# Kernel tuning notes

Hardware: AMD Instinct MI355X
Metric: run time of the kernel (lower is better)

The kernel has to match this reference:

```python
import jax, jax.numpy as jnp
import numpy as np

B, S, DM, H = 4, 1024, 1024, 16
D = DM // H  # attn_head_size = 64


def setup_inputs() -> dict:
    key = jax.random.key(0)
    ks = jax.random.split(key, 16)
    sc = 0.02
    return {
        "hidden_states": jax.random.normal(ks[0], (B, S, DM), jnp.float32),
        "wq": jax.random.normal(ks[1], (DM, DM), jnp.float32) * sc,
        "bq": jax.random.normal(ks[2], (DM,), jnp.float32) * sc,
        "wk": jax.random.normal(ks[3], (DM, DM), jnp.float32) * sc,
        "bk": jax.random.normal(ks[4], (DM,), jnp.float32) * sc,
        "wv": jax.random.normal(ks[5], (DM, DM), jnp.float32) * sc,
        "bv": jax.random.normal(ks[6], (DM,), jnp.float32) * sc,
        "wo": jax.random.normal(ks[7], (DM, DM), jnp.float32) * sc,
        "bo": jax.random.normal(ks[8], (DM,), jnp.float32) * sc,
        "wfq": jax.random.normal(ks[9], (DM, DM), jnp.float32) * sc,
        "bfq": jax.random.normal(ks[10], (DM,), jnp.float32) * sc,
        "wfg": jax.random.normal(ks[11], (DM, DM), jnp.float32) * sc,
        "bfg": jax.random.normal(ks[12], (DM,), jnp.float32) * sc,
        "up": jax.random.normal(ks[13], (H, 1, D), jnp.float32) * sc,
        "uz": jax.random.normal(ks[14], (H, 1, D), jnp.float32) * sc,
    }


def _split_heads(x):
    # [B, S, DM] -> [B, H, S, D]
    return x.reshape(x.shape[0], x.shape[1], H, D).transpose(0, 2, 1, 3)


def reference(hidden_states, wq, bq, wk, bk, wv, bv, wo, bo,
              wfq, bfq, wfg, bfg, up, uz):
    key_len = hidden_states.shape[1]
    mixed_q = hidden_states @ wq + bq  # [B, S, DM]
    mixed_k = hidden_states @ wk + bk
    mixed_v = hidden_states @ wv + bv

    # focus-attention Gaussian bias
    glo = jnp.mean(mixed_q, axis=1, keepdims=True)                      # [B, 1, DM]
    c = jnp.tanh((mixed_q @ wfq + bfq) + (glo @ wfg + bfg))             # [B, S, DM]
    c = _split_heads(c)                                                 # [B, H, S, D]
    p = jnp.sum(c * up[None], axis=-1)                                  # [B, H, S]
    z = jnp.sum(c * uz[None], axis=-1)                                  # [B, H, S]
    P = jax.nn.sigmoid(p) * key_len                                     # [B, H, S]
    Z = jax.nn.sigmoid(z) * key_len
    j = jnp.arange(key_len, dtype=P.dtype)                              # [S]
    # G[b,h,q,k] = -(k - P[b,h,q])^2 * 2 / Z[b,h,q]^2
    G = -((j[None, None, None, :] - P[..., None]) ** 2) * 2.0 / (Z[..., None] ** 2)

    q = _split_heads(mixed_q)
    k = _split_heads(mixed_k)
    v = _split_heads(mixed_v)

    scores = jnp.einsum("bhqd,bhkd->bhqk", q, k) / jnp.sqrt(jnp.float32(D))
    scores = scores + G
    probs = jax.nn.softmax(scores, axis=-1)  # dropout_prob = 0 -> no-op
    ctx = jnp.einsum("bhqk,bhkd->bhqd", probs, v)
    ctx = ctx.transpose(0, 2, 1, 3).reshape(ctx.shape[0], key_len, H * D)
    return ctx @ wo + bo
```

## Files before the change

### kernel.cpp

```cpp
#include <hip/hip_runtime.h>
#include <hip/hip_bf16.h>
#include <stdint.h>

#define DEV __device__ __forceinline__

typedef __attribute__((ext_vector_type(4))) float f32x4;
typedef __attribute__((ext_vector_type(8))) __bf16 bf16x8;
typedef __attribute__((ext_vector_type(4))) __bf16 bf16x4;
typedef __attribute__((ext_vector_type(4))) unsigned int uint4v;
typedef __attribute__((ext_vector_type(4))) int i32x4;

static constexpr int Bc = 4, Sc = 1024, DMc = 1024, Hc = 16, Dh = 64;
static constexpr int Mc = Bc * Sc;

DEV __bf16 f2b(float x) {
    unsigned u = __builtin_bit_cast(unsigned, x);
    unsigned r = (u + 0x7fffu + ((u >> 16) & 1u)) >> 16;
    return __builtin_bit_cast(__bf16, (unsigned short)r);
}
DEV float b2f(__bf16 x) {
    unsigned short s = __builtin_bit_cast(unsigned short, x);
    unsigned u = ((unsigned)s) << 16;
    return __builtin_bit_cast(float, u);
}
DEV unsigned cvt_pk_bf16(float a, float b) {
    unsigned r;
    asm("v_cvt_pk_bf16_f32 %0, %1, %2" : "=v"(r) : "v"(a), "v"(b));
    return r;
}
DEV void gload_lds16(const void* g, void* l) {
    __builtin_amdgcn_global_load_lds(
        (const __attribute__((address_space(1))) unsigned int*)g,
        (__attribute__((address_space(3))) unsigned int*)l,
        16, 0, 0);
}
DEV bf16x8 ldswz(const __bf16* base, int row, int cu) {
    const char* p = (const char*)base + row * 128 + (((cu) ^ (row & 7)) << 4);
    return *(const bf16x8*)p;
}

__global__ void k_cvt2(const float* __restrict__ hs, __bf16* __restrict__ hsb,
                       float* __restrict__ part0) {
    int sc = blockIdx.x, b = blockIdx.y, tid = threadIdx.x;
    int c0 = tid * 4;
    float4 s = {0.f, 0.f, 0.f, 0.f};
#pragma unroll
    for (int r = 0; r < 8; r++) {
        size_t row = (size_t)b * 1024 + sc * 8 + r;
        float4 v = *(const float4*)&hs[row * 1024 + c0];
        s.x += v.x; s.y += v.y; s.z += v.z; s.w += v.w;
        bf16x4 o = { f2b(v.x), f2b(v.y), f2b(v.z), f2b(v.w) };
        *(bf16x4*)&hsb[row * 1024 + c0] = o;
    }
    *(float4*)&part0[(size_t)(sc * 4 + b) * 1024 + c0] = s;
}

__global__ void k_tcvt5(const float* __restrict__ s0, const float* __restrict__ s1,
                        const float* __restrict__ s2, const float* __restrict__ s3,
                        const float* __restrict__ s4,
                        __bf16* __restrict__ d0, __bf16* __restrict__ d1,
                        __bf16* __restrict__ d2, __bf16* __restrict__ d3,
                        __bf16* __restrict__ d4, __bf16* __restrict__ wqb) {
    __shared__ float t[32][33];
    const float* in; __bf16* out;
    switch (blockIdx.z) {
        case 0: in = s0; out = d0; break;
        case 1: in = s1; out = d1; break;
        case 2: in = s2; out = d2; break;
        case 3: in = s3; out = d3; break;
        default: in = s4; out = d4; break;
    }
    int c0 = blockIdx.x * 32, r0 = blockIdx.y * 32;
    for (int j = 0; j < 4; j++) {
        float v = in[(size_t)(r0 + threadIdx.y + j * 8) * 1024 + c0 + threadIdx.x];
        t[threadIdx.y + j * 8][threadIdx.x] = v;
        if (blockIdx.z == 0)
            wqb[(size_t)(r0 + threadIdx.y + j * 8) * 1024 + c0 + threadIdx.x] = f2b(v);
    }
    __syncthreads();
    for (int j = 0; j < 4; j++)
        out[(size_t)(c0 + threadIdx.y + j * 8) * 1024 + r0 + threadIdx.x] = f2b(t[threadIdx.x][threadIdx.y + j * 8]);
}

template <int EPI, int BM>
__global__ __launch_bounds__(256) void k_gemm(
    const __bf16* __restrict__ A, const __bf16* __restrict__ Bt,
    const float* __restrict__ bias, void* __restrict__ Cout, int N, int K)
{
    constexpr int MF = BM / 32;
    constexpr int ACH = BM / 32;
    __shared__ __bf16 Al[2][BM * 64];
    __shared__ __bf16 Bl[2][128 * 64];
    const int bm = blockIdx.x, bn = blockIdx.y;
    const int tid = threadIdx.x, lane = tid & 63, wid = tid >> 6;
    const int l15 = lane & 15, lg = lane >> 4;
    const int qr = (wid >> 1) * (BM / 2), qc = (wid & 1) * 64;
    f32x4 acc[MF][4] = {};

    const __bf16* Ab = A + (size_t)bm * BM * K;
    const __bf16* Bb = Bt + (size_t)bn * 128 * K;

#pragma unroll
    for (int c = 0; c < ACH; c++) {
        int ch = c * 256 + tid, row = ch >> 3, cu = (ch & 7) ^ (row & 7);
        gload_lds16(&Ab[(size_t)row * K + cu * 8], &Al[0][ch * 8]);
    }
#pragma unroll
    for (int c = 0; c < 4; c++) {
        int ch = c * 256 + tid, row = ch >> 3, cu = (ch & 7) ^ (row & 7);
        gload_lds16(&Bb[(size_t)row * K + cu * 8], &Bl[0][ch * 8]);
    }
    asm volatile("s_waitcnt vmcnt(0)" ::: "memory");
    __builtin_amdgcn_s_barrier();

    int buf = 0;
    for (int t = 0; t < K / 64; t++) {
        if (t + 1 < K / 64) {
            int k0 = (t + 1) * 64;
#pragma unroll
            for (int c = 0; c < ACH; c++) {
                int ch = c * 256 + tid, row = ch >> 3, cu = (ch & 7) ^ (row & 7);
                gload_lds16(&Ab[(size_t)row * K + k0 + cu * 8], &Al[buf ^ 1][ch * 8]);
            }
#pragma unroll
            for (int c = 0; c < 4; c++) {
                int ch = c * 256 + tid, row = ch >> 3, cu = (ch & 7) ^ (row & 7);
                gload_lds16(&Bb[(size_t)row * K + k0 + cu * 8], &Bl[buf ^ 1][ch * 8]);
            }
        }
        bf16x8 af[MF][2], bfv[4][2];
#pragma unroll
        for (int m = 0; m < MF; m++)
#pragma unroll
            for (int ks = 0; ks < 2; ks++) af[m][ks] = ldswz(&Al[buf][0], qr + m * 16 + l15, ks * 4 + lg);
#pragma unroll
        for (int n = 0; n < 4; n++)
#pragma unroll
            for (int ks = 0; ks < 2; ks++) bfv[n][ks] = ldswz(&Bl[buf][0], qc + n * 16 + l15, ks * 4 + lg);
#pragma unroll
        for (int m = 0; m < MF; m++)
#pragma unroll
            for (int n = 0; n < 4; n++) {
                acc[m][n] = __builtin_amdgcn_mfma_f32_16x16x32_bf16(af[m][0], bfv[n][0], acc[m][n], 0, 0, 0);
                acc[m][n] = __builtin_amdgcn_mfma_f32_16x16x32_bf16(af[m][1], bfv[n][1], acc[m][n], 0, 0, 0);
            }
        asm volatile("s_waitcnt vmcnt(0)" ::: "memory");
        __builtin_amdgcn_s_barrier();
        buf ^= 1;
    }
#pragma unroll
    for (int m = 0; m < MF; m++) {
        int row_base = bm * BM + qr + m * 16 + lg * 4;
#pragma unroll
        for (int n = 0; n < 4; n++) {
            int col = bn * 128 + qc + n * 16 + l15;
            float bsum = bias ? bias[col] : 0.0f;
#pragma unroll
            for (int r = 0; r < 4; r++) {
                int row = row_base + r;
                float v = acc[m][n][r] + bsum;
                if constexpr (EPI == 2) ((float*)Cout)[(size_t)row * N + col] = v;
                else ((__bf16*)Cout)[(size_t)row * N + col] = f2b(v);
            }
        }
    }
}

__global__ __launch_bounds__(256) void k_qkvc(
    const __bf16* __restrict__ A, const __bf16* __restrict__ BtAll,
    const float* __restrict__ bq, const float* __restrict__ bk, const float* __restrict__ bv,
    const float* __restrict__ gt2, const float* __restrict__ up, const float* __restrict__ uz,
    __bf16* __restrict__ mq, __bf16* __restrict__ mk_, __bf16* __restrict__ vt,
    float* __restrict__ Pf, float* __restrict__ Zf)
{
    constexpr int K = 1024;
    __shared__ __bf16 Al[2][128 * 64];
    __shared__ __bf16 Bl[2][128 * 64];
    const int bm = blockIdx.x, bn = blockIdx.y;
    const int tid = threadIdx.x, lane = tid & 63, wid = tid >> 6;
    const int l15 = lane & 15, lg = lane >> 4;
    const int qr = (wid >> 1) * 64, qc = (wid & 1) * 64;
    f32x4 acc[4][4] = {};

    const __bf16* Ab = A + (size_t)bm * 128 * K;
    const __bf16* Bb = BtAll + (size_t)bn * 128 * K;

#pragma unroll
    for (int c = 0; c < 4; c++) {
        int ch = c * 256 + tid, row = ch >> 3, cu = (ch & 7) ^ (row & 7);
        gload_lds16(&Ab[(size_t)row * K + cu * 8], &Al[0][ch * 8]);
        gload_lds16(&Bb[(size_t)row * K + cu * 8], &Bl[0][ch * 8]);
    }
    asm volatile("s_waitcnt vmcnt(0)" ::: "memory");
    __builtin_amdgcn_s_barrier();

    int buf = 0;
    for (int t = 0; t < 16; t++) {
        if (t < 15) {
            int k0 = (t + 1) * 64;
#pragma unroll
            for (int c = 0; c < 4; c++) {
                int ch = c * 256 + tid, row = ch >> 3, cu = (ch & 7) ^ (row & 7);
                gload_lds16(&Ab[(size_t)row * K + k0 + cu * 8], &Al[buf ^ 1][ch * 8]);
                gload_lds16(&Bb[(size_t)row * K + k0 + cu * 8], &Bl[buf ^ 1][ch * 8]);
            }
        }
        bf16x8 af[4][2], bfv[4][2];
#pragma unroll
        for (int m = 0; m < 4; m++)
#pragma unroll
            for (int ks = 0; ks < 2; ks++) af[m][ks] = ldswz(&Al[buf][0], qr + m * 16 + l15, ks * 4 + lg);
#pragma unroll
        for (int n = 0; n < 4; n++)
#pragma unroll
            for (int ks = 0; ks < 2; ks++) bfv[n][ks] = ldswz(&Bl[buf][0], qc + n * 16 + l15, ks * 4 + lg);
#pragma unroll
        for (int m = 0; m < 4; m++)
#pragma unroll
            for (int n = 0; n < 4; n++) {
                acc[m][n] = __builtin_amdgcn_mfma_f32_16x16x32_bf16(af[m][0], bfv[n][0], acc[m][n], 0, 0, 0);
                acc[m][n] = __builtin_amdgcn_mfma_f32_16x16x32_bf16(af[m][1], bfv[n][1], acc[m][n], 0, 0, 0);
            }
        asm volatile("s_waitcnt vmcnt(0)" ::: "memory");
        __builtin_amdgcn_s_barrier();
        buf ^= 1;
    }

    const int chunk = bn >> 3;
    if (chunk == 3) {
        const int h = (bn & 7) * 2 + (qc >> 6);
        float upv[4], uzv[4];
#pragma unroll
        for (int n = 0; n < 4; n++) {
            upv[n] = up[h * 64 + n * 16 + l15];
            uzv[n] = uz[h * 64 + n * 16 + l15];
        }
#pragma unroll
        for (int m = 0; m < 4; m++) {
            int row_base = bm * 128 + qr + m * 16 + lg * 4;
#pragma unroll
            for (int r = 0; r < 4; r++) {
                int row = row_base + r;
                float p = 0.f, z = 0.f;
#pragma unroll
                for (int n = 0; n < 4; n++) {
                    int col = (bn & 7) * 128 + qc + n * 16 + l15;
                    float cv = tanhf(acc[m][n][r] + gt2[(row >> 10) * 1024 + col]);
                    p += cv * upv[n];
                    z += cv * uzv[n];
                }
#pragma unroll
                for (int d = 1; d < 16; d <<= 1) {
                    p += __shfl_xor(p, d, 16);
                    z += __shfl_xor(z, d, 16);
                }
                if (l15 == 0) {
                    int bb = row >> 10, s = row & 1023;
                    Pf[((size_t)(bb * 16 + h)) * 1024 + s] = 1024.f / (1.f + __expf(-p));
                    Zf[((size_t)(bb * 16 + h)) * 1024 + s] = 1024.f / (1.f + __expf(-z));
                }
            }
        }
    } else if (chunk == 2) {
        const int b = bm >> 3;
#pragma unroll
        for (int m = 0; m < 4; m++) {
            int s0 = (bm & 7) * 128 + qr + m * 16 + lg * 4;
#pragma unroll
            for (int n = 0; n < 4; n++) {
                int col = (bn & 7) * 128 + qc + n * 16 + l15;
                int h = col >> 6, d = col & 63;
                float bsum = bv[col];
                bf16x4 o = { f2b(acc[m][n][0] + bsum), f2b(acc[m][n][1] + bsum),
                             f2b(acc[m][n][2] + bsum), f2b(acc[m][n][3] + bsum) };
                *(bf16x4*)&vt[((size_t)((b * 16 + h) * 64 + d)) * 1024 + s0] = o;
            }
        }
    } else {
        const float* bias = chunk == 0 ? bq : bk;
        __bf16* outp = chunk == 0 ? mq : mk_;
#pragma unroll
        for (int m = 0; m < 4; m++) {
            int row_base = bm * 128 + qr + m * 16 + lg * 4;
#pragma unroll
            for (int n = 0; n < 4; n++) {
                int col = (bn & 7) * 128 + qc + n * 16 + l15;
                float bsum = bias[col];
#pragma unroll
                for (int r = 0; r < 4; r++) {
                    int row = row_base + r;
                    outp[(size_t)row * 1024 + col] = f2b(acc[m][n][r] + bsum);
                }
            }
        }
    }
}

__global__ void k_glo2(const float* __restrict__ part0, const float* __restrict__ wq,
                       float* __restrict__ glo_part) {
    __shared__ float ghs_l[256];
    int tid = threadIdx.x, kc = blockIdx.y;
    {
        int bb = tid >> 6, kk = tid & 63, k = kc * 64 + kk;
        float s = 0.f;
        for (int sc = 0; sc < 128; sc++) s += part0[(size_t)(sc * 4 + bb) * 1024 + k];
        ghs_l[tid] = s * (1.0f / 1024.f);
    }
    __syncthreads();
    int n = blockIdx.x * 256 + tid;
    float a0 = 0, a1 = 0, a2 = 0, a3 = 0;
    for (int j = 0; j < 64; j++) {
        float w = wq[(size_t)(kc * 64 + j) * 1024 + n];
        a0 += ghs_l[j] * w; a1 += ghs_l[64 + j] * w; a2 += ghs_l[128 + j] * w; a3 += ghs_l[192 + j] * w;
    }
    glo_part[(kc * 4 + 0) * 1024 + n] = a0;
    glo_part[(kc * 4 + 1) * 1024 + n] = a1;
    glo_part[(kc * 4 + 2) * 1024 + n] = a2;
    glo_part[(kc * 4 + 3) * 1024 + n] = a3;
}
__global__ void k_gt2p(const float* __restrict__ glo_part, const float* __restrict__ bq,
                       const float* __restrict__ wfg, const float* __restrict__ wfq,
                       float* __restrict__ gt_part) {
    __shared__ float glo_l[256];
    int tid = threadIdx.x, kc = blockIdx.y;
    {
        int bb = tid >> 6, kk = tid & 63, k = kc * 64 + kk;
        float s = bq[k];
        for (int k2 = 0; k2 < 16; k2++) s += glo_part[(k2 * 4 + bb) * 1024 + k];
        glo_l[tid] = s;
    }
    __syncthreads();
    int n = blockIdx.x * 256 + tid;
    float a0 = 0, a1 = 0, a2 = 0, a3 = 0, t = 0;
    for (int j = 0; j < 64; j++) {
        int k = kc * 64 + j;
        float wg = wfg[(size_t)k * 1024 + n];
        float wf = wfq[(size_t)k * 1024 + n];
        a0 += glo_l[j] * wg; a1 += glo_l[64 + j] * wg; a2 += glo_l[128 + j] * wg; a3 += glo_l[192 + j] * wg;
        t += bq[k] * wf;
    }
    gt_part[(kc * 4 + 0) * 1024 + n] = a0 + t;
    gt_part[(kc * 4 + 1) * 1024 + n] = a1 + t;
    gt_part[(kc * 4 + 2) * 1024 + n] = a2 + t;
    gt_part[(kc * 4 + 3) * 1024 + n] = a3 + t;
}
__global__ void k_red_gt(const float* __restrict__ gt_part, const float* __restrict__ bfg,
                         const float* __restrict__ bfq, float* __restrict__ gt2) {
    int i = blockIdx.x * 256 + threadIdx.x;
    int b = i >> 10, n = i & 1023;
    float s = bfg[n] + bfq[n];
    for (int kc = 0; kc < 16; kc++) s += gt_part[(kc * 4 + b) * 1024 + n];
    gt2[i] = s;
}

DEV bf16x8 ldfrag(const __bf16* base, int row, int colbyte) {
    const char* p = (const char*)base + (size_t)row * 128 + (colbyte ^ ((row & 7) << 4));
    return *(const bf16x8*)p;
}

__global__ __launch_bounds__(256) void k_attn(
    const __bf16* __restrict__ Q, const __bf16* __restrict__ Kx, const __bf16* __restrict__ Vt_g,
    const float* __restrict__ Pf, const float* __restrict__ Zf, __bf16* __restrict__ ctx)
{
    __shared__ __bf16 Kl[2][64 * 64];
    __shared__ __bf16 Vl[2][64 * 64];
    const int qt = blockIdx.x, h = blockIdx.y, b = blockIdx.z;
    const int tid = threadIdx.x, lane = tid & 63, wid = tid >> 6;
    const int l15 = lane & 15, lg = lane >> 4;
    const int qbase = qt * 128 + wid * 32;
    const size_t qoff = ((size_t)(b * Sc)) * DMc + h * Dh;

    bf16x8 qf[2][2];
#pragma unroll
    for (int qh = 0; qh < 2; qh++)
#pragma unroll
        for (int dh = 0; dh < 2; dh++)
            qf[qh][dh] = *(const bf16x8*)&Q[qoff + (size_t)(qbase + qh * 16 + l15) * DMc + dh * 32 + lg * 8];

    float Pr[2], Ar[2];
#pragma unroll
    for (int qh = 0; qh < 2; qh++) {
        int row = qbase + qh * 16 + l15;
        float pp = Pf[((size_t)(b * 16 + h)) * 1024 + row];
        float zz = Zf[((size_t)(b * 16 + h)) * 1024 + row];
        Pr[qh] = pp; Ar[qh] = 2.0f / (zz * zz);
    }
    float l[2] = {0.f, 0.f};
    f32x4 oacc[2][4] = {};

    const __bf16* Kbase = Kx + qoff;
    const __bf16* Vbase = Vt_g + ((size_t)((b * 16 + h) * 64)) * 1024;

#pragma unroll
    for (int i = 0; i < 2; i++) {
        int ch = i * 256 + tid, row = ch >> 3, off = ch & 7;
        uint4v kv = *(const uint4v*)&Kbase[(size_t)row * DMc + off * 8];
        uint4v vv = *(const uint4v*)&Vbase[(size_t)row * 1024 + off * 8];
        *(uint4v*)((char*)&Kl[0][0] + row * 128 + ((off * 16) ^ ((row & 7) << 4))) = kv;
        *(uint4v*)((char*)&Vl[0][0] + row * 128 + ((off * 16) ^ ((row & 7) << 4))) = vv;
    }
    __syncthreads();

    for (int t = 0; t < 16; t++) {
        const int buf = t & 1;
        uint4v rk[2], rv[2];
        if (t < 15) {
#pragma unroll
            for (int i = 0; i < 2; i++) {
                int ch = i * 256 + tid, row = ch >> 3, off = ch & 7;
                rk[i] = *(const uint4v*)&Kbase[(size_t)((t + 1) * 64 + row) * DMc + off * 8];
                rv[i] = *(const uint4v*)&Vbase[(size_t)row * 1024 + (t + 1) * 64 + off * 8];
            }
        }

        f32x4 st[2][4];
        __builtin_amdgcn_s_setprio(1);
#pragma unroll
        for (int c = 0; c < 4; c++) {
            bf16x8 kb0 = ldfrag(&Kl[buf][0], c * 16 + l15, lg * 16);
            bf16x8 kb1 = ldfrag(&Kl[buf][0], c * 16 + l15, 64 + lg * 16);
#pragma unroll
            for (int qh = 0; qh < 2; qh++) {
                f32x4 a = {0.f, 0.f, 0.f, 0.f};
                a = __builtin_amdgcn_mfma_f32_16x16x32_bf16(kb0, qf[qh][0], a, 0, 0, 0);
                a = __builtin_amdgcn_mfma_f32_16x16x32_bf16(kb1, qf[qh][1], a, 0, 0, 0);
                st[qh][c] = a;
            }
        }
        __builtin_amdgcn_s_setprio(0);

        int pk[2][4][2];
#pragma unroll
        for (int qh = 0; qh < 2; qh++) {
            float s[16];
#pragma unroll
            for (int c = 0; c < 4; c++)
#pragma unroll
                for (int r = 0; r < 4; r++) {
                    float kidx = (float)(t * 64 + c * 16 + lg * 4 + r);
                    float dk = kidx - Pr[qh];
                    s[c * 4 + r] = __expf(st[qh][c][r] * 0.125f - dk * dk * Ar[qh]);
                }
            float rs = 0.f;
#pragma unroll
            for (int i = 0; i < 16; i++) rs += s[i];
            rs += __shfl_xor(rs, 16, 64);
            rs += __shfl_xor(rs, 32, 64);
            l[qh] += rs;
#pragma unroll
            for (int c = 0; c < 4; c++) {
                pk[qh][c][0] = (int)cvt_pk_bf16(s[c * 4 + 0], s[c * 4 + 1]);
                pk[qh][c][1] = (int)cvt_pk_bf16(s[c * 4 + 2], s[c * 4 + 3]);
            }
        }

        const int a0 = (((lg & 1) << 1) * 16 + l15) * 4;
        const int a1 = a0 + 64;
        const int selhi = lg >> 1;
#pragma unroll
        for (int kh = 0; kh < 2; kh++) {
            bf16x8 vb[4];
#pragma unroll
            for (int dt = 0; dt < 4; dt++) vb[dt] = ldfrag(&Vl[buf][0], dt * 16 + l15, kh * 64 + lg * 16);
#pragma unroll
            for (int qh = 0; qh < 2; qh++) {
                int w[4];
#pragma unroll
                for (int wi = 0; wi < 4; wi++) {
                    int addr = (wi < 2) ? a0 : a1;
                    int pr = wi & 1;
                    int va = __builtin_amdgcn_ds_bpermute(addr, pk[qh][kh * 2 + 0][pr]);
                    int vb2 = __builtin_amdgcn_ds_bpermute(addr, pk[qh][kh * 2 + 1][pr]);
                    w[wi] = selhi ? vb2 : va;
                }
                i32x4 wv = {w[0], w[1], w[2], w[3]};
                bf16x8 pa = __builtin_bit_cast(bf16x8, wv);
                __builtin_amdgcn_s_setprio(1);
#pragma unroll
                for (int dt = 0; dt < 4; dt++)
                    oacc[qh][dt] = __builtin_amdgcn_mfma_f32_16x16x32_bf16(pa, vb[dt], oacc[qh][dt], 0, 0, 0);
                __builtin_amdgcn_s_setprio(0);
            }
        }

        if (t < 15) {
#pragma unroll
            for (int i = 0; i < 2; i++) {
                int ch = i * 256 + tid, row = ch >> 3, off = ch & 7;
                *(uint4v*)((char*)&Kl[buf ^ 1][0] + row * 128 + ((off * 16) ^ ((row & 7) << 4))) = rk[i];
                *(uint4v*)((char*)&Vl[buf ^ 1][0] + row * 128 + ((off * 16) ^ ((row & 7) << 4))) = rv[i];
            }
        }
        __syncthreads();
    }

#pragma unroll
    for (int qh = 0; qh < 2; qh++) {
        float lr[4];
#pragma unroll
        for (int r = 0; r < 4; r++) lr[r] = __shfl(l[qh], lg * 4 + r, 16);
#pragma unroll
        for (int dt = 0; dt < 4; dt++)
#pragma unroll
            for (int r = 0; r < 4; r++) {
                int row = qbase + qh * 16 + lg * 4 + r;
                ctx[((size_t)(b * Sc) + row) * DMc + h * Dh + dt * 16 + l15] =
                    f2b(oacc[qh][dt][r] / lr[r]);
            }
    }
}

extern "C" void kernel_launch(void* const* d_in, const int* in_sizes, int n_in,
                              void* d_out, int out_size, void* d_ws, size_t ws_size,
                              hipStream_t stream) {
    const float* hs  = (const float*)d_in[0];
    const float* wq  = (const float*)d_in[1];
    const float* bq  = (const float*)d_in[2];
    const float* wk  = (const float*)d_in[3];
    const float* bk  = (const float*)d_in[4];
    const float* wv  = (const float*)d_in[5];
    const float* bv  = (const float*)d_in[6];
    const float* wo  = (const float*)d_in[7];
    const float* bo  = (const float*)d_in[8];
    const float* wfq = (const float*)d_in[9];
    const float* bfq = (const float*)d_in[10];
    const float* wfg = (const float*)d_in[11];
    const float* bfg = (const float*)d_in[12];
    const float* up  = (const float*)d_in[13];
    const float* uz  = (const float*)d_in[14];

    char* ws = (char*)d_ws;
    const size_t MB = 1ull << 20;
    __bf16* hsb   = (__bf16*)(ws);
    __bf16* BtAll = (__bf16*)(ws + 8 * MB);
    __bf16* wfqT  = (__bf16*)(ws + 16 * MB);
    __bf16* woT   = (__bf16*)(ws + 18 * MB);
    __bf16* mq    = (__bf16*)(ws + 20 * MB);
    __bf16* mk    = (__bf16*)(ws + 28 * MB);
    __bf16* vt    = (__bf16*)(ws + 36 * MB);
    __bf16* ctxb  = (__bf16*)(ws);
    __bf16* wqb   = (__bf16*)(ws + 55 * MB);
    char* sm = ws + 52 * MB;
    float* Pf       = (float*)(sm);
    float* Zf       = (float*)(sm + (256 << 10));
    float* glo_part = (float*)(sm + (512 << 10));
    float* gt_part  = (float*)(sm + (768 << 10));
    float* gt2      = (float*)(sm + (1024 << 10));
    float* part0    = (float*)(ws + 57 * MB);

    k_cvt2<<<dim3(128, 4), 256, 0, stream>>>(hs, hsb, part0);
    k_tcvt5<<<dim3(32, 32, 5), dim3(32, 8), 0, stream>>>(
        wq, wk, wv, wfq, wo,
        BtAll, BtAll + 1048576, BtAll + 2097152, wfqT, woT, wqb);

    k_glo2<<<dim3(4, 16), 256, 0, stream>>>(part0, wq, glo_part);
    k_gt2p<<<dim3(4, 16), 256, 0, stream>>>(glo_part, bq, wfg, wfq, gt_part);
    k_red_gt<<<16, 256, 0, stream>>>(gt_part, bfg, bfq, gt2);

    k_gemm<0, 64><<<dim3(16, 8), 256, 0, stream>>>(wfqT, wqb, nullptr, BtAll + 3145728, DMc, DMc);

    k_qkvc<<<dim3(32, 32), 256, 0, stream>>>(hsb, BtAll, bq, bk, bv, gt2, up, uz,
                                             mq, mk, vt, Pf, Zf);

    k_attn<<<dim3(8, 16, 4), 256, 0, stream>>>(mq, mk, vt, Pf, Zf, ctxb);

    k_gemm<2, 64><<<dim3(64, 8), 256, 0, stream>>>(ctxb, woT, bo, d_out, DMc, DMc);
}
```

Measured before the change: 168.6 us.

## Double KV tile size per pipeline stage in attention kernel

```diff
diff --git a/kernel.cpp b/kernel.cpp
--- a/kernel.cpp
+++ b/kernel.cpp
@@ -353,8 +353,12 @@
     gt2[i] = s;
 }
 
-DEV bf16x8 ldfrag(const __bf16* base, int row, int colbyte) {
+DEV bf16x8 ldfragK(const __bf16* base, int row, int colbyte) {
     const char* p = (const char*)base + (size_t)row * 128 + (colbyte ^ ((row & 7) << 4));
+    return *(const bf16x8*)p;
+}
+DEV bf16x8 ldfragV(const __bf16* base, int row, int colbyte) {
+    const char* p = (const char*)base + (size_t)row * 256 + (colbyte ^ ((row & 15) << 4));
     return *(const bf16x8*)p;
 }
 
@@ -362,8 +366,8 @@
     const __bf16* __restrict__ Q, const __bf16* __restrict__ Kx, const __bf16* __restrict__ Vt_g,
     const float* __restrict__ Pf, const float* __restrict__ Zf, __bf16* __restrict__ ctx)
 {
-    __shared__ __bf16 Kl[2][64 * 64];
-    __shared__ __bf16 Vl[2][64 * 64];
+    __shared__ __bf16 Kl[2][128 * 64];
+    __shared__ __bf16 Vl[2][64 * 128];
     const int qt = blockIdx.x, h = blockIdx.y, b = blockIdx.z;
     const int tid = threadIdx.x, lane = tid & 63, wid = tid >> 6;
     const int l15 = lane & 15, lg = lane >> 4;
@@ -392,103 +396,117 @@
     const __bf16* Vbase = Vt_g + ((size_t)((b * 16 + h) * 64)) * 1024;
 
 #pragma unroll
-    for (int i = 0; i < 2; i++) {
-        int ch = i * 256 + tid, row = ch >> 3, off = ch & 7;
-        uint4v kv = *(const uint4v*)&Kbase[(size_t)row * DMc + off * 8];
-        uint4v vv = *(const uint4v*)&Vbase[(size_t)row * 1024 + off * 8];
-        *(uint4v*)((char*)&Kl[0][0] + row * 128 + ((off * 16) ^ ((row & 7) << 4))) = kv;
-        *(uint4v*)((char*)&Vl[0][0] + row * 128 + ((off * 16) ^ ((row & 7) << 4))) = vv;
+    for (int i = 0; i < 4; i++) {
+        int ch = i * 256 + tid;
+        {
+            int row = ch >> 3, off = ch & 7;
+            uint4v kv = *(const uint4v*)&Kbase[(size_t)row * DMc + off * 8];
+            *(uint4v*)((char*)&Kl[0][0] + row * 128 + ((off * 16) ^ ((row & 7) << 4))) = kv;
+        }
+        {
+            int row = ch >> 4, off = ch & 15;
+            uint4v vv = *(const uint4v*)&Vbase[(size_t)row * 1024 + off * 8];
+            *(uint4v*)((char*)&Vl[0][0] + row * 256 + ((off * 16) ^ ((row & 15) << 4))) = vv;
+        }
     }
     __syncthreads();
 
-    for (int t = 0; t < 16; t++) {
+    for (int t = 0; t < 8; t++) {
         const int buf = t & 1;
-        uint4v rk[2], rv[2];
-        if (t < 15) {
-#pragma unroll
-            for (int i = 0; i < 2; i++) {
-                int ch = i * 256 + tid, row = ch >> 3, off = ch & 7;
-                rk[i] = *(const uint4v*)&Kbase[(size_t)((t + 1) * 64 + row) * DMc + off * 8];
-                rv[i] = *(const uint4v*)&Vbase[(size_t)row * 1024 + (t + 1) * 64 + off * 8];
-            }
-        }
-
-        f32x4 st[2][4];
-        __builtin_amdgcn_s_setprio(1);
-#pragma unroll
-        for (int c = 0; c < 4; c++) {
-            bf16x8 kb0 = ldfrag(&Kl[buf][0], c * 16 + l15, lg * 16);
-            bf16x8 kb1 = ldfrag(&Kl[buf][0], c * 16 + l15, 64 + lg * 16);
+        uint4v rk[4], rv[4];
+        if (t < 7) {
+#pragma unroll
+            for (int i = 0; i < 4; i++) {
+                int ch = i * 256 + tid;
+                int krow = ch >> 3, koff = ch & 7;
+                rk[i] = *(const uint4v*)&Kbase[(size_t)((t + 1) * 128 + krow) * DMc + koff * 8];
+                int vrow = ch >> 4, voff = ch & 15;
+                rv[i] = *(const uint4v*)&Vbase[(size_t)vrow * 1024 + (t + 1) * 128 + voff * 8];
+            }
+        }
+
+#pragma unroll
+        for (int sub = 0; sub < 2; sub++) {
+            f32x4 st[2][4];
+            __builtin_amdgcn_s_setprio(1);
+#pragma unroll
+            for (int c = 0; c < 4; c++) {
+                bf16x8 kb0 = ldfragK(&Kl[buf][0], sub * 64 + c * 16 + l15, lg * 16);
+                bf16x8 kb1 = ldfragK(&Kl[buf][0], sub * 64 + c * 16 + l15, 64 + lg * 16);
+#pragma unroll
+                for (int qh = 0; qh < 2; qh++) {
+                    f32x4 a = {0.f, 0.f, 0.f, 0.f};
+                    a = __builtin_amdgcn_mfma_f32_16x16x32_bf16(kb0, qf[qh][0], a, 0, 0, 0);
+                    a = __builtin_amdgcn_mfma_f32_16x16x32_bf16(kb1, qf[qh][1], a, 0, 0, 0);
+                    st[qh][c] = a;
+                }
+            }
+            __builtin_amdgcn_s_setprio(0);
+
+            int pk[2][4][2];
 #pragma unroll
             for (int qh = 0; qh < 2; qh++) {
-                f32x4 a = {0.f, 0.f, 0.f, 0.f};
-                a = __builtin_amdgcn_mfma_f32_16x16x32_bf16(kb0, qf[qh][0], a, 0, 0, 0);
-                a = __builtin_amdgcn_mfma_f32_16x16x32_bf16(kb1, qf[qh][1], a, 0, 0, 0);
-                st[qh][c] = a;
-            }
-        }
-        __builtin_amdgcn_s_setprio(0);
-
-        int pk[2][4][2];
-#pragma unroll
-        for (int qh = 0; qh < 2; qh++) {
-            float s[16];
-#pragma unroll
-            for (int c = 0; c < 4; c++)
-#pragma unroll
-                for (int r = 0; r < 4; r++) {
-                    float kidx = (float)(t * 64 + c * 16 + lg * 4 + r);
-                    float dk = kidx - Pr[qh];
-                    s[c * 4 + r] = __expf(st[qh][c][r] * 0.125f - dk * dk * Ar[qh]);
-                }
-            float rs = 0.f;
-#pragma unroll
-            for (int i = 0; i < 16; i++) rs += s[i];
-            rs += __shfl_xor(rs, 16, 64);
-            rs += __shfl_xor(rs, 32, 64);
-            l[qh] += rs;
-#pragma unroll
-            for (int c = 0; c < 4; c++) {
-                pk[qh][c][0] = (int)cvt_pk_bf16(s[c * 4 + 0], s[c * 4 + 1]);
-                pk[qh][c][1] = (int)cvt_pk_bf16(s[c * 4 + 2], s[c * 4 + 3]);
-            }
-        }
-
-        const int a0 = (((lg & 1) << 1) * 16 + l15) * 4;
-        const int a1 = a0 + 64;
-        const int selhi = lg >> 1;
-#pragma unroll
-        for (int kh = 0; kh < 2; kh++) {
-            bf16x8 vb[4];
-#pragma unroll
-            for (int dt = 0; dt < 4; dt++) vb[dt] = ldfrag(&Vl[buf][0], dt * 16 + l15, kh * 64 + lg * 16);
-#pragma unroll
-            for (int qh = 0; qh < 2; qh++) {
-                int w[4];
-#pragma unroll
-                for (int wi = 0; wi < 4; wi++) {
-                    int addr = (wi < 2) ? a0 : a1;
-                    int pr = wi & 1;
-                    int va = __builtin_amdgcn_ds_bpermute(addr, pk[qh][kh * 2 + 0][pr]);
-                    int vb2 = __builtin_amdgcn_ds_bpermute(addr, pk[qh][kh * 2 + 1][pr]);
-                    w[wi] = selhi ? vb2 : va;
-                }
-                i32x4 wv = {w[0], w[1], w[2], w[3]};
-                bf16x8 pa = __builtin_bit_cast(bf16x8, wv);
-                __builtin_amdgcn_s_setprio(1);
+                float s[16];
+#pragma unroll
+                for (int c = 0; c < 4; c++)
+#pragma unroll
+                    for (int r = 0; r < 4; r++) {
+                        float kidx = (float)(t * 128 + sub * 64 + c * 16 + lg * 4 + r);
+                        float dk = kidx - Pr[qh];
+                        s[c * 4 + r] = __expf(st[qh][c][r] * 0.125f - dk * dk * Ar[qh]);
+                    }
+                float rs = 0.f;
+#pragma unroll
+                for (int i = 0; i < 16; i++) rs += s[i];
+                rs += __shfl_xor(rs, 16, 64);
+                rs += __shfl_xor(rs, 32, 64);
+                l[qh] += rs;
+#pragma unroll
+                for (int c = 0; c < 4; c++) {
+                    pk[qh][c][0] = (int)cvt_pk_bf16(s[c * 4 + 0], s[c * 4 + 1]);
+                    pk[qh][c][1] = (int)cvt_pk_bf16(s[c * 4 + 2], s[c * 4 + 3]);
+                }
+            }
+
+            const int a0 = (((lg & 1) << 1) * 16 + l15) * 4;
+            const int a1 = a0 + 64;
+            const int selhi = lg >> 1;
+#pragma unroll
+            for (int kh = 0; kh < 2; kh++) {
+                bf16x8 vb[4];
 #pragma unroll
                 for (int dt = 0; dt < 4; dt++)
-                    oacc[qh][dt] = __builtin_amdgcn_mfma_f32_16x16x32_bf16(pa, vb[dt], oacc[qh][dt], 0, 0, 0);
-                __builtin_amdgcn_s_setprio(0);
-            }
-        }
-
-        if (t < 15) {
-#pragma unroll
-            for (int i = 0; i < 2; i++) {
-                int ch = i * 256 + tid, row = ch >> 3, off = ch & 7;
-                *(uint4v*)((char*)&Kl[buf ^ 1][0] + row * 128 + ((off * 16) ^ ((row & 7) << 4))) = rk[i];
-                *(uint4v*)((char*)&Vl[buf ^ 1][0] + row * 128 + ((off * 16) ^ ((row & 7) << 4))) = rv[i];
+                    vb[dt] = ldfragV(&Vl[buf][0], dt * 16 + l15, sub * 128 + kh * 64 + lg * 16);
+#pragma unroll
+                for (int qh = 0; qh < 2; qh++) {
+                    int w[4];
+#pragma unroll
+                    for (int wi = 0; wi < 4; wi++) {
+                        int addr = (wi < 2) ? a0 : a1;
+                        int pr = wi & 1;
+                        int va = __builtin_amdgcn_ds_bpermute(addr, pk[qh][kh * 2 + 0][pr]);
+                        int vb2 = __builtin_amdgcn_ds_bpermute(addr, pk[qh][kh * 2 + 1][pr]);
+                        w[wi] = selhi ? vb2 : va;
+                    }
+                    i32x4 wv = {w[0], w[1], w[2], w[3]};
+                    bf16x8 pa = __builtin_bit_cast(bf16x8, wv);
+                    __builtin_amdgcn_s_setprio(1);
+#pragma unroll
+                    for (int dt = 0; dt < 4; dt++)
+                        oacc[qh][dt] = __builtin_amdgcn_mfma_f32_16x16x32_bf16(pa, vb[dt], oacc[qh][dt], 0, 0, 0);
+                    __builtin_amdgcn_s_setprio(0);
+                }
+            }
+        }
+
+        if (t < 7) {
+#pragma unroll
+            for (int i = 0; i < 4; i++) {
+                int ch = i * 256 + tid;
+                int krow = ch >> 3, koff = ch & 7;
+                *(uint4v*)((char*)&Kl[buf ^ 1][0] + krow * 128 + ((koff * 16) ^ ((krow & 7) << 4))) = rk[i];
+                int vrow = ch >> 4, voff = ch & 15;
+                *(uint4v*)((char*)&Vl[buf ^ 1][0] + vrow * 256 + ((voff * 16) ^ ((vrow & 15) << 4))) = rv[i];
             }
         }
         __syncthreads();
```

Measured after the change: 174.1 us. +3.3%, slower.
